# Kernel tuning notes

Hardware: AMD Instinct MI355X
Metric: run time of the kernel (lower is better)

## Reference

```python
import jax, jax.numpy as jnp
import numpy as np

# Model constants (match init_kwargs / torchcde conventions)
B = 1024        # batch
L = 128         # number of spline knots (grid_points = 0..L-1)
C_IN = 8        # input_channels
HID = 64        # hidden_channels
MLP_H = 128     # CDEFunc hidden width
INIT_H = 20     # initial-network hidden width


def setup_inputs() -> dict:
    key = jax.random.key(0)
    ks = jax.random.split(key, 9)
    # cubic spline coeffs: (B, L-1, 4*C_IN) laid out as [a, b, c, d] per interval
    coeffs = jax.random.normal(ks[0], (B, L - 1, 4 * C_IN), dtype=jnp.float32) * 0.1
    # initial network: C_IN -> 20 -> HID (ReLU, then Tanh)
    Wi1 = jax.random.normal(ks[1], (C_IN, INIT_H), dtype=jnp.float32) / np.sqrt(C_IN)
    bi1 = jnp.zeros((INIT_H,), jnp.float32)
    Wi2 = jax.random.normal(ks[2], (INIT_H, HID), dtype=jnp.float32) / np.sqrt(INIT_H)
    bi2 = jnp.zeros((HID,), jnp.float32)
    # CDE vector field: (HID+1) -> 128 -> C_IN*HID (ReLU, then Tanh)
    W1 = jax.random.normal(ks[3], (HID + 1, MLP_H), dtype=jnp.float32) / np.sqrt(HID + 1)
    b1 = jnp.zeros((MLP_H,), jnp.float32)
    W2 = jax.random.normal(ks[4], (MLP_H, C_IN * HID), dtype=jnp.float32) / np.sqrt(MLP_H)
    b2 = jnp.zeros((C_IN * HID,), jnp.float32)
    return {"coeffs": coeffs, "Wi1": Wi1, "bi1": bi1, "Wi2": Wi2, "bi2": bi2,
            "W1": W1, "b1": b1, "W2": W2, "b2": b2}


def reference(coeffs, Wi1, bi1, Wi2, bi2, W1, b1, W2, b2):
    Lm1 = coeffs.shape[1]
    # a,b,c,d: each (B, L-1, C_IN). X(t) = a + b*f + c*f^2 + d*f^3 on interval idx,
    # dX/dt = b + 2c*f + 3d*f^2, with f = t - idx (torchcde CubicSpline convention).
    a, b, c, d = jnp.split(coeffs, 4, axis=-1)

    def dXdt(t):
        idx = jnp.clip(jnp.floor(t).astype(jnp.int32), 0, Lm1 - 1)
        fr = t - idx
        return b[:, idx] + 2.0 * c[:, idx] * fr + 3.0 * d[:, idx] * fr * fr  # (B, C_IN)

    def cde_func(t, z):
        # FFN([HID+1, 128, C_IN*HID], ReLU hidden, Tanh output) on concat(t, z)
        tz = jnp.concatenate([jnp.full((z.shape[0], 1), t, z.dtype), z], axis=1)
        h = jax.nn.relu(tz @ W1 + b1)
        return jnp.tanh(h @ W2 + b2).reshape(z.shape[0], HID, C_IN)  # (B, HID, C_IN)

    def vf(t, z):
        # dz/dt = f(t,z) @ dX/dt
        return jnp.einsum('bhc,bc->bh', cde_func(t, z), dXdt(t))

    # z0 = initial(X(t0)); X(0) = a at interval 0 with frac 0
    X0 = a[:, 0]
    z0 = jnp.tanh(jax.nn.relu(X0 @ Wi1 + bi1) @ Wi2 + bi2)  # (B, HID)

    def rk4_step(z, i):
        t = i.astype(z.dtype)
        k1 = vf(t, z)
        k2 = vf(t + 0.5, z + 0.5 * k1)
        k3 = vf(t + 0.5, z + 0.5 * k2)
        k4 = vf(t + 1.0, z + k3)
        z_new = z + (k1 + 2.0 * k2 + 2.0 * k3 + k4) / 6.0
        return z_new, z_new

    _, zs = jax.lax.scan(rk4_step, z0, jnp.arange(Lm1))  # (L-1, B, HID)
    # z evaluated at all grid points, like cdeint(t=X.grid_points): (B, L, HID)
    return jnp.concatenate([z0[None], zs], axis=0).transpose(1, 0, 2)
```

## Files before the change

kernel.cpp:

```cpp
#include <hip/hip_runtime.h>
#include <stdint.h>

#define LM1  127
#define NTHR 512

typedef _Float16 half8_t __attribute__((ext_vector_type(8)));
typedef _Float16 half4_t __attribute__((ext_vector_type(4)));
typedef float    f32x4   __attribute__((ext_vector_type(4)));

__device__ __forceinline__ float fast_tanh(float x) {
  float e = __expf(2.0f * x);
  return 1.0f - 2.0f * __builtin_amdgcn_rcpf(e + 1.0f);
}

#define BAR() asm volatile("s_waitcnt lgkmcnt(0)\n\ts_barrier" ::: "memory")

__global__ void __launch_bounds__(NTHR, 2) cde_kernel(
    const float* __restrict__ coeffs,
    const float* __restrict__ Wi1, const float* __restrict__ bi1,
    const float* __restrict__ Wi2, const float* __restrict__ bi2,
    const float* __restrict__ W1,  const float* __restrict__ b1,
    const float* __restrict__ W2,  const float* __restrict__ b2,
    float* __restrict__ out)
{
  __shared__ __align__(16) _Float16 zsbT[2][1024];
  __shared__ __align__(16) _Float16 hA[2048];
  __shared__ __align__(16) float    gds[2][3][4][8];

  const int t    = threadIdx.x;
  const int lane = t & 63;
  const int w    = t >> 6;
  const int l15  = lane & 15;
  const int lq   = lane >> 4;
  const int lqh  = lq >> 1, lql = lq & 1;
  const int r4   = l15 & 3;
  const bool rowok = (l15 < 4);
  const int row0 = blockIdx.x * 4;

  for (int u = t; u < 1024; u += NTHR) ((uint32_t*)zsbT)[u] = 0u;

  half8_t wA[2];
  #pragma unroll
  for (int kt = 0; kt < 2; ++kt)
    #pragma unroll
    for (int j = 0; j < 8; ++j)
      wA[kt][j] = (_Float16)W1[(1 + 32 * kt + 8 * lq + j) * 128 + 16 * w + l15];

  f32x4 w1t4, b14;
  #pragma unroll
  for (int reg = 0; reg < 4; ++reg) {
    w1t4[reg] = W1[16 * w + 4 * lq + reg];
    b14[reg]  = b1[16 * w + 4 * lq + reg];
  }

  half8_t wf[4][4];
  #pragma unroll
  for (int mt = 0; mt < 4; ++mt)
    #pragma unroll
    for (int kt = 0; kt < 4; ++kt)
      #pragma unroll
      for (int j = 0; j < 8; ++j)
        wf[mt][kt][j] =
            (_Float16)W2[(32 * kt + 8 * lq + j) * 512 + 64 * w + 16 * mt + l15];

  f32x4 b2v[4];
  #pragma unroll
  for (int mt = 0; mt < 4; ++mt)
    b2v[mt] = *(const f32x4*)&b2[64 * w + 16 * mt + 4 * lq];

  _Float16* const hwp = &hA[128 * (2 * w + lqh) + 8 * l15 + 4 * lql];
  const int zbase = 128 * w + 8 * l15;
  const int dA = 4 * lql + lqh;
  const int dB = 4 * lql + 2 + lqh;

  float z[4];
  {
    const float* cb = coeffs + (size_t)(row0 + r4) * (LM1 * 32);
    float x0[8];
    #pragma unroll
    for (int c = 0; c < 8; ++c) x0[c] = cb[c];
    float acc[4];
    #pragma unroll
    for (int mt = 0; mt < 4; ++mt) acc[mt] = bi2[8 * w + 2 * mt + lqh];
    for (int j = 0; j < 20; ++j) {
      float uj = bi1[j];
      #pragma unroll
      for (int c = 0; c < 8; ++c) uj += x0[c] * Wi1[c * 20 + j];
      uj = fmaxf(uj, 0.0f);
      #pragma unroll
      for (int mt = 0; mt < 4; ++mt) acc[mt] += uj * Wi2[j * 64 + 8 * w + 2 * mt + lqh];
    }
    #pragma unroll
    for (int mt = 0; mt < 4; ++mt) z[mt] = fast_tanh(acc[mt]);
  }
  if (rowok) {
    const float zA = lql ? z[2] : z[0];
    const float zB = lql ? z[3] : z[1];
    zsbT[0][zbase + dA] = (_Float16)zA;
    zsbT[0][zbase + dB] = (_Float16)zB;
    float* op = out + (size_t)(row0 + l15) * 8192 + 8 * w;
    op[dA] = zA;
    op[dB] = zB;
  }

  const int rg = (lane >> 3) & 3, cg = lane & 7;
  const float* cbp = coeffs + (size_t)(row0 + rg) * (LM1 * 32);
  float pb = 0.f, pc = 0.f, pd = 0.f, pbn = 0.f;
  const bool stg = (w == 7) && (lane < 32);
  if (stg) { pb = cbp[8 + cg]; pc = cbp[16 + cg]; pd = cbp[24 + cg]; pbn = cbp[40 + cg]; }

  __syncthreads();

  for (int i = 0; i < LM1; ++i) {
    if (stg) {
      gds[i & 1][0][rg][cg] = pb;
      gds[i & 1][1][rg][cg] = pb + pc + 0.75f * pd;
      gds[i & 1][2][rg][cg] = (i < LM1 - 1) ? pbn : fmaf(3.0f, pd, fmaf(2.0f, pc, pb));
      if (i + 1 < LM1) {
        const float* nb = cbp + (size_t)(i + 1) * 32;
        pb = nb[8 + cg]; pc = nb[16 + cg]; pd = nb[24 + cg];
        pbn = (i + 2 < LM1) ? nb[40 + cg] : 0.0f;
      }
    }

    float ksum[4] = {0.f, 0.f, 0.f, 0.f};
    #pragma unroll
    for (int s = 0; s < 4; ++s) {
      const int   rb = s & 1, wb = rb ^ 1;
      const int   gi = (s == 0) ? 0 : (s == 3) ? 2 : 1;
      const float ts = (float)i + ((s == 0) ? 0.0f : (s == 3) ? 1.0f : 0.5f);

      const half8_t zb0 = *(const half8_t*)(&zsbT[rb][8 * lane]);
      const half8_t zb1 = *(const half8_t*)(&zsbT[rb][512 + 8 * lane]);
      f32x4 hd = {0.f, 0.f, 0.f, 0.f};
      hd = __builtin_amdgcn_mfma_f32_16x16x32_f16(wA[0], zb0, hd, 0, 0, 0);
      hd = __builtin_amdgcn_mfma_f32_16x16x32_f16(wA[1], zb1, hd, 0, 0, 0);
      half4_t hv;
      hv[0] = (_Float16)fmaxf(hd.x + fmaf(ts, w1t4.x, b14.x), 0.0f);
      hv[1] = (_Float16)fmaxf(hd.y + fmaf(ts, w1t4.y, b14.y), 0.0f);
      hv[2] = (_Float16)fmaxf(hd.z + fmaf(ts, w1t4.z, b14.z), 0.0f);
      hv[3] = (_Float16)fmaxf(hd.w + fmaf(ts, w1t4.w, b14.w), 0.0f);
      *(half4_t*)hwp = hv;
      BAR();

      const f32x4 gv = *(const f32x4*)&gds[i & 1][gi][r4][4 * lql];
      half8_t hb[4];
      #pragma unroll
      for (int kt = 0; kt < 4; ++kt)
        hb[kt] = *(const half8_t*)(&hA[512 * kt + 8 * lane]);
      f32x4 d0 = {0.f, 0.f, 0.f, 0.f}, d1 = d0, d2 = d0, d3 = d0;
      #pragma unroll
      for (int kt = 0; kt < 4; ++kt) {
        d0 = __builtin_amdgcn_mfma_f32_16x16x32_f16(wf[0][kt], hb[kt], d0, 0, 0, 0);
        d1 = __builtin_amdgcn_mfma_f32_16x16x32_f16(wf[1][kt], hb[kt], d1, 0, 0, 0);
        d2 = __builtin_amdgcn_mfma_f32_16x16x32_f16(wf[2][kt], hb[kt], d2, 0, 0, 0);
        d3 = __builtin_amdgcn_mfma_f32_16x16x32_f16(wf[3][kt], hb[kt], d3, 0, 0, 0);
      }
      const float p0 = fast_tanh(d0.x + b2v[0].x) * gv.x + fast_tanh(d0.y + b2v[0].y) * gv.y
                     + fast_tanh(d0.z + b2v[0].z) * gv.z + fast_tanh(d0.w + b2v[0].w) * gv.w;
      const float p1 = fast_tanh(d1.x + b2v[1].x) * gv.x + fast_tanh(d1.y + b2v[1].y) * gv.y
                     + fast_tanh(d1.z + b2v[1].z) * gv.z + fast_tanh(d1.w + b2v[1].w) * gv.w;
      const float p2 = fast_tanh(d2.x + b2v[2].x) * gv.x + fast_tanh(d2.y + b2v[2].y) * gv.y
                     + fast_tanh(d2.z + b2v[2].z) * gv.z + fast_tanh(d2.w + b2v[2].w) * gv.w;
      const float p3 = fast_tanh(d3.x + b2v[3].x) * gv.x + fast_tanh(d3.y + b2v[3].y) * gv.y
                     + fast_tanh(d3.z + b2v[3].z) * gv.z + fast_tanh(d3.w + b2v[3].w) * gv.w;
      const float kcv0 = p0 + __shfl_xor(p0, 16, 64);
      const float kcv1 = p1 + __shfl_xor(p1, 16, 64);
      const float kcv2 = p2 + __shfl_xor(p2, 16, 64);
      const float kcv3 = p3 + __shfl_xor(p3, 16, 64);
      const float wgt = (s == 1 || s == 2) ? 2.0f : 1.0f;
      ksum[0] += wgt * kcv0;
      ksum[1] += wgt * kcv1;
      ksum[2] += wgt * kcv2;
      ksum[3] += wgt * kcv3;

      if (s < 3) {
        const float cn = (s == 2) ? 1.0f : 0.5f;
        if (rowok) {
          const float zA = lql ? z[2] : z[0], kA = lql ? kcv2 : kcv0;
          const float zB = lql ? z[3] : z[1], kB = lql ? kcv3 : kcv1;
          zsbT[wb][zbase + dA] = (_Float16)fmaf(cn, kA, zA);
          zsbT[wb][zbase + dB] = (_Float16)fmaf(cn, kB, zB);
        }
      } else {
        z[0] = fmaf(ksum[0], 1.0f / 6.0f, z[0]);
        z[1] = fmaf(ksum[1], 1.0f / 6.0f, z[1]);
        z[2] = fmaf(ksum[2], 1.0f / 6.0f, z[2]);
        z[3] = fmaf(ksum[3], 1.0f / 6.0f, z[3]);
        if (rowok) {
          const float zA = lql ? z[2] : z[0];
          const float zB = lql ? z[3] : z[1];
          zsbT[wb][zbase + dA] = (_Float16)zA;
          zsbT[wb][zbase + dB] = (_Float16)zB;
          float* op = out + (size_t)(row0 + l15) * 8192 + (size_t)(i + 1) * 64 + 8 * w;
          op[dA] = zA;
          op[dB] = zB;
        }
      }
      BAR();
    }
  }
}

extern "C" void kernel_launch(void* const* d_in, const int* in_sizes, int n_in,
                              void* d_out, int out_size, void* d_ws, size_t ws_size,
                              hipStream_t stream) {
  const float* coeffs = (const float*)d_in[0];
  const float* Wi1    = (const float*)d_in[1];
  const float* bi1    = (const float*)d_in[2];
  const float* Wi2    = (const float*)d_in[3];
  const float* bi2    = (const float*)d_in[4];
  const float* W1     = (const float*)d_in[5];
  const float* b1     = (const float*)d_in[6];
  const float* W2     = (const float*)d_in[7];
  const float* b2     = (const float*)d_in[8];
  float* out          = (float*)d_out;
  (void)in_sizes; (void)n_in; (void)out_size; (void)d_ws; (void)ws_size;
  cde_kernel<<<256, NTHR, 0, stream>>>(coeffs, Wi1, bi1, Wi2, bi2,
                                       W1, b1, W2, b2, out);
}
```

Before: 605.0 us.

## Halve block to 4 waves, compute full hidden layer per wave to drop mid-stage barrier

Shrinks the block from 8 to 4 waves and has each wave compute the whole 128-wide first MLP layer redundantly into a private LDS buffer. This removes one of the two block barriers per RK stage. Each wave now owns 128 output columns of the second layer (8 MFMA tiles instead of 4), and spline-coefficient staging moves to the end of the last stage. The cost is redundant first-layer MFMA work, much higher register pressure from holding 8x2 plus 8x4 weight fragments, and fewer waves for latency hiding, with launch bounds dropped to 1 block.

```diff
diff --git a/kernel.cpp b/kernel.cpp
--- a/kernel.cpp
+++ b/kernel.cpp
@@ -2,7 +2,7 @@
 #include <stdint.h>
 
 #define LM1  127
-#define NTHR 512
+#define NTHR 256
 
 typedef _Float16 half8_t __attribute__((ext_vector_type(8)));
 typedef _Float16 half4_t __attribute__((ext_vector_type(4)));
@@ -15,7 +15,7 @@
 
 #define BAR() asm volatile("s_waitcnt lgkmcnt(0)\n\ts_barrier" ::: "memory")
 
-__global__ void __launch_bounds__(NTHR, 2) cde_kernel(
+__global__ void __launch_bounds__(NTHR, 1) cde_kernel(
     const float* __restrict__ coeffs,
     const float* __restrict__ Wi1, const float* __restrict__ bi1,
     const float* __restrict__ Wi2, const float* __restrict__ bi2,
@@ -24,7 +24,7 @@
     float* __restrict__ out)
 {
   __shared__ __align__(16) _Float16 zsbT[2][1024];
-  __shared__ __align__(16) _Float16 hA[2048];
+  __shared__ __align__(16) _Float16 hA[4][2048];
   __shared__ __align__(16) float    gds[2][3][4][8];
 
   const int t    = threadIdx.x;
@@ -34,96 +34,106 @@
   const int lq   = lane >> 4;
   const int lqh  = lq >> 1, lql = lq & 1;
   const int r4   = l15 & 3;
-  const bool rowok = (l15 < 4);
+  const bool owner = (l15 < 4) && (lql == 0);
   const int row0 = blockIdx.x * 4;
 
   for (int u = t; u < 1024; u += NTHR) ((uint32_t*)zsbT)[u] = 0u;
 
-  half8_t wA[2];
-  #pragma unroll
-  for (int kt = 0; kt < 2; ++kt)
-    #pragma unroll
-    for (int j = 0; j < 8; ++j)
-      wA[kt][j] = (_Float16)W1[(1 + 32 * kt + 8 * lq + j) * 128 + 16 * w + l15];
-
-  f32x4 w1t4, b14;
-  #pragma unroll
-  for (int reg = 0; reg < 4; ++reg) {
-    w1t4[reg] = W1[16 * w + 4 * lq + reg];
-    b14[reg]  = b1[16 * w + 4 * lq + reg];
-  }
-
-  half8_t wf[4][4];
-  #pragma unroll
-  for (int mt = 0; mt < 4; ++mt)
+  half8_t wA[8][2];
+  #pragma unroll
+  for (int m = 0; m < 8; ++m)
+    #pragma unroll
+    for (int kt = 0; kt < 2; ++kt)
+      #pragma unroll
+      for (int j = 0; j < 8; ++j)
+        wA[m][kt][j] = (_Float16)W1[(1 + 32 * kt + 8 * lq + j) * 128 + 16 * m + l15];
+
+  f32x4 w1t4[8], b14[8];
+  #pragma unroll
+  for (int m = 0; m < 8; ++m)
+    #pragma unroll
+    for (int reg = 0; reg < 4; ++reg) {
+      w1t4[m][reg] = W1[16 * m + 4 * lq + reg];
+      b14[m][reg]  = b1[16 * m + 4 * lq + reg];
+    }
+
+  half8_t wf[8][4];
+  #pragma unroll
+  for (int mt = 0; mt < 8; ++mt)
     #pragma unroll
     for (int kt = 0; kt < 4; ++kt)
       #pragma unroll
       for (int j = 0; j < 8; ++j)
         wf[mt][kt][j] =
-            (_Float16)W2[(32 * kt + 8 * lq + j) * 512 + 64 * w + 16 * mt + l15];
-
-  f32x4 b2v[4];
-  #pragma unroll
-  for (int mt = 0; mt < 4; ++mt)
-    b2v[mt] = *(const f32x4*)&b2[64 * w + 16 * mt + 4 * lq];
-
-  _Float16* const hwp = &hA[128 * (2 * w + lqh) + 8 * l15 + 4 * lql];
-  const int zbase = 128 * w + 8 * l15;
-  const int dA = 4 * lql + lqh;
-  const int dB = 4 * lql + 2 + lqh;
-
-  float z[4];
+            (_Float16)W2[(32 * kt + 8 * lq + j) * 512 + 128 * w + 16 * mt + l15];
+
+  f32x4 b2v[8];
+  #pragma unroll
+  for (int mt = 0; mt < 8; ++mt)
+    b2v[mt] = *(const f32x4*)&b2[128 * w + 16 * mt + 4 * lq];
+
+  _Float16* const hAp = &hA[w][0];
+  const int hbase = 8 * l15 + 4 * lql + 128 * lqh;
+
+  int zoffs[8];
+  #pragma unroll
+  for (int mt = 0; mt < 8; ++mt) {
+    const int h = 16 * w + 2 * mt + lqh;
+    zoffs[mt] = 512 * (h >> 5) + 128 * ((h >> 3) & 3) + 8 * l15 + (h & 7);
+  }
+
+  float z[8];
   {
     const float* cb = coeffs + (size_t)(row0 + r4) * (LM1 * 32);
     float x0[8];
     #pragma unroll
     for (int c = 0; c < 8; ++c) x0[c] = cb[c];
-    float acc[4];
-    #pragma unroll
-    for (int mt = 0; mt < 4; ++mt) acc[mt] = bi2[8 * w + 2 * mt + lqh];
+    float acc[8];
+    #pragma unroll
+    for (int mt = 0; mt < 8; ++mt) acc[mt] = bi2[16 * w + 2 * mt + lqh];
     for (int j = 0; j < 20; ++j) {
       float uj = bi1[j];
       #pragma unroll
       for (int c = 0; c < 8; ++c) uj += x0[c] * Wi1[c * 20 + j];
       uj = fmaxf(uj, 0.0f);
       #pragma unroll
-      for (int mt = 0; mt < 4; ++mt) acc[mt] += uj * Wi2[j * 64 + 8 * w + 2 * mt + lqh];
-    }
-    #pragma unroll
-    for (int mt = 0; mt < 4; ++mt) z[mt] = fast_tanh(acc[mt]);
-  }
-  if (rowok) {
-    const float zA = lql ? z[2] : z[0];
-    const float zB = lql ? z[3] : z[1];
-    zsbT[0][zbase + dA] = (_Float16)zA;
-    zsbT[0][zbase + dB] = (_Float16)zB;
-    float* op = out + (size_t)(row0 + l15) * 8192 + 8 * w;
-    op[dA] = zA;
-    op[dB] = zB;
+      for (int mt = 0; mt < 8; ++mt) acc[mt] += uj * Wi2[j * 64 + 16 * w + 2 * mt + lqh];
+    }
+    #pragma unroll
+    for (int mt = 0; mt < 8; ++mt) z[mt] = fast_tanh(acc[mt]);
+  }
+  if (owner) {
+    #pragma unroll
+    for (int mt = 0; mt < 8; ++mt) {
+      zsbT[0][zoffs[mt]] = (_Float16)z[mt];
+      out[(size_t)(row0 + l15) * 8192 + 16 * w + 2 * mt + lqh] = z[mt];
+    }
   }
 
   const int rg = (lane >> 3) & 3, cg = lane & 7;
   const float* cbp = coeffs + (size_t)(row0 + rg) * (LM1 * 32);
-  float pb = 0.f, pc = 0.f, pd = 0.f, pbn = 0.f;
-  const bool stg = (w == 7) && (lane < 32);
-  if (stg) { pb = cbp[8 + cg]; pc = cbp[16 + cg]; pd = cbp[24 + cg]; pbn = cbp[40 + cg]; }
+  const bool stg = (w == 3) && (lane < 32);
+  float pb2 = 0.f, pc2 = 0.f, pd2 = 0.f, pbn2 = 0.f;
+  if (stg) {
+    const float pb = cbp[8 + cg], pc = cbp[16 + cg], pd = cbp[24 + cg], pbn = cbp[40 + cg];
+    gds[0][0][rg][cg] = pb;
+    gds[0][1][rg][cg] = pb + pc + 0.75f * pd;
+    gds[0][2][rg][cg] = pbn;
+  }
 
   __syncthreads();
 
   for (int i = 0; i < LM1; ++i) {
-    if (stg) {
-      gds[i & 1][0][rg][cg] = pb;
-      gds[i & 1][1][rg][cg] = pb + pc + 0.75f * pd;
-      gds[i & 1][2][rg][cg] = (i < LM1 - 1) ? pbn : fmaf(3.0f, pd, fmaf(2.0f, pc, pb));
-      if (i + 1 < LM1) {
-        const float* nb = cbp + (size_t)(i + 1) * 32;
-        pb = nb[8 + cg]; pc = nb[16 + cg]; pd = nb[24 + cg];
-        pbn = (i + 2 < LM1) ? nb[40 + cg] : 0.0f;
-      }
-    }
-
-    float ksum[4] = {0.f, 0.f, 0.f, 0.f};
+    if (stg && i + 1 < LM1) {
+      const float* nb = cbp + (size_t)(i + 1) * 32;
+      pb2 = nb[8 + cg]; pc2 = nb[16 + cg]; pd2 = nb[24 + cg];
+      pbn2 = (i + 2 < LM1) ? nb[40 + cg] : 0.0f;
+    }
+
+    float ksum[8];
+    #pragma unroll
+    for (int mt = 0; mt < 8; ++mt) ksum[mt] = 0.0f;
+
     #pragma unroll
     for (int s = 0; s < 4; ++s) {
       const int   rb = s & 1, wb = rb ^ 1;
@@ -132,70 +142,62 @@
 
       const half8_t zb0 = *(const half8_t*)(&zsbT[rb][8 * lane]);
       const half8_t zb1 = *(const half8_t*)(&zsbT[rb][512 + 8 * lane]);
-      f32x4 hd = {0.f, 0.f, 0.f, 0.f};
-      hd = __builtin_amdgcn_mfma_f32_16x16x32_f16(wA[0], zb0, hd, 0, 0, 0);
-      hd = __builtin_amdgcn_mfma_f32_16x16x32_f16(wA[1], zb1, hd, 0, 0, 0);
-      half4_t hv;
-      hv[0] = (_Float16)fmaxf(hd.x + fmaf(ts, w1t4.x, b14.x), 0.0f);
-      hv[1] = (_Float16)fmaxf(hd.y + fmaf(ts, w1t4.y, b14.y), 0.0f);
-      hv[2] = (_Float16)fmaxf(hd.z + fmaf(ts, w1t4.z, b14.z), 0.0f);
-      hv[3] = (_Float16)fmaxf(hd.w + fmaf(ts, w1t4.w, b14.w), 0.0f);
-      *(half4_t*)hwp = hv;
-      BAR();
-
       const f32x4 gv = *(const f32x4*)&gds[i & 1][gi][r4][4 * lql];
+
+      #pragma unroll
+      for (int m = 0; m < 8; ++m) {
+        f32x4 hd = {0.f, 0.f, 0.f, 0.f};
+        hd = __builtin_amdgcn_mfma_f32_16x16x32_f16(wA[m][0], zb0, hd, 0, 0, 0);
+        hd = __builtin_amdgcn_mfma_f32_16x16x32_f16(wA[m][1], zb1, hd, 0, 0, 0);
+        half4_t hv;
+        hv[0] = (_Float16)fmaxf(hd.x + fmaf(ts, w1t4[m].x, b14[m].x), 0.0f);
+        hv[1] = (_Float16)fmaxf(hd.y + fmaf(ts, w1t4[m].y, b14[m].y), 0.0f);
+        hv[2] = (_Float16)fmaxf(hd.z + fmaf(ts, w1t4[m].z, b14[m].z), 0.0f);
+        hv[3] = (_Float16)fmaxf(hd.w + fmaf(ts, w1t4[m].w, b14[m].w), 0.0f);
+        *(half4_t*)(hAp + hbase + 256 * m) = hv;
+      }
+      asm volatile("s_waitcnt lgkmcnt(0)" ::: "memory");
+
       half8_t hb[4];
       #pragma unroll
       for (int kt = 0; kt < 4; ++kt)
-        hb[kt] = *(const half8_t*)(&hA[512 * kt + 8 * lane]);
-      f32x4 d0 = {0.f, 0.f, 0.f, 0.f}, d1 = d0, d2 = d0, d3 = d0;
-      #pragma unroll
-      for (int kt = 0; kt < 4; ++kt) {
-        d0 = __builtin_amdgcn_mfma_f32_16x16x32_f16(wf[0][kt], hb[kt], d0, 0, 0, 0);
-        d1 = __builtin_amdgcn_mfma_f32_16x16x32_f16(wf[1][kt], hb[kt], d1, 0, 0, 0);
-        d2 = __builtin_amdgcn_mfma_f32_16x16x32_f16(wf[2][kt], hb[kt], d2, 0, 0, 0);
-        d3 = __builtin_amdgcn_mfma_f32_16x16x32_f16(wf[3][kt], hb[kt], d3, 0, 0, 0);
+        hb[kt] = *(const half8_t*)(hAp + 512 * kt + 8 * lane);
+      f32x4 d[8];
+      #pragma unroll
+      for (int mt = 0; mt < 8; ++mt) d[mt] = (f32x4){0.f, 0.f, 0.f, 0.f};
+      #pragma unroll
+      for (int kt = 0; kt < 4; ++kt)
+        #pragma unroll
+        for (int mt = 0; mt < 8; ++mt)
+          d[mt] = __builtin_amdgcn_mfma_f32_16x16x32_f16(wf[mt][kt], hb[kt], d[mt], 0, 0, 0);
+
+      const float wgt = (s == 1 || s == 2) ? 2.0f : 1.0f;
+      const float cn  = (s == 2) ? 1.0f : 0.5f;
+      #pragma unroll
+      for (int mt = 0; mt < 8; ++mt) {
+        float p = fast_tanh(d[mt].x + b2v[mt].x) * gv.x
+                + fast_tanh(d[mt].y + b2v[mt].y) * gv.y
+                + fast_tanh(d[mt].z + b2v[mt].z) * gv.z
+                + fast_tanh(d[mt].w + b2v[mt].w) * gv.w;
+        const float kcv = p + __shfl_xor(p, 16, 64);
+        ksum[mt] += wgt * kcv;
+        if (s < 3) {
+          if (owner) zsbT[wb][zoffs[mt]] = (_Float16)fmaf(cn, kcv, z[mt]);
+        } else {
+          z[mt] = fmaf(ksum[mt], 1.0f / 6.0f, z[mt]);
+          if (owner) {
+            zsbT[wb][zoffs[mt]] = (_Float16)z[mt];
+            out[(size_t)(row0 + l15) * 8192 + (size_t)(i + 1) * 64
+                + 16 * w + 2 * mt + lqh] = z[mt];
+          }
+        }
       }
-      const float p0 = fast_tanh(d0.x + b2v[0].x) * gv.x + fast_tanh(d0.y + b2v[0].y) * gv.y
-                     + fast_tanh(d0.z + b2v[0].z) * gv.z + fast_tanh(d0.w + b2v[0].w) * gv.w;
-      const float p1 = fast_tanh(d1.x + b2v[1].x) * gv.x + fast_tanh(d1.y + b2v[1].y) * gv.y
-                     + fast_tanh(d1.z + b2v[1].z) * gv.z + fast_tanh(d1.w + b2v[1].w) * gv.w;
-      const float p2 = fast_tanh(d2.x + b2v[2].x) * gv.x + fast_tanh(d2.y + b2v[2].y) * gv.y
-                     + fast_tanh(d2.z + b2v[2].z) * gv.z + fast_tanh(d2.w + b2v[2].w) * gv.w;
-      const float p3 = fast_tanh(d3.x + b2v[3].x) * gv.x + fast_tanh(d3.y + b2v[3].y) * gv.y
-                     + fast_tanh(d3.z + b2v[3].z) * gv.z + fast_tanh(d3.w + b2v[3].w) * gv.w;
-      const float kcv0 = p0 + __shfl_xor(p0, 16, 64);
-      const float kcv1 = p1 + __shfl_xor(p1, 16, 64);
-      const float kcv2 = p2 + __shfl_xor(p2, 16, 64);
-      const float kcv3 = p3 + __shfl_xor(p3, 16, 64);
-      const float wgt = (s == 1 || s == 2) ? 2.0f : 1.0f;
-      ksum[0] += wgt * kcv0;
-      ksum[1] += wgt * kcv1;
-      ksum[2] += wgt * kcv2;
-      ksum[3] += wgt * kcv3;
-
-      if (s < 3) {
-        const float cn = (s == 2) ? 1.0f : 0.5f;
-        if (rowok) {
-          const float zA = lql ? z[2] : z[0], kA = lql ? kcv2 : kcv0;
-          const float zB = lql ? z[3] : z[1], kB = lql ? kcv3 : kcv1;
-          zsbT[wb][zbase + dA] = (_Float16)fmaf(cn, kA, zA);
-          zsbT[wb][zbase + dB] = (_Float16)fmaf(cn, kB, zB);
-        }
-      } else {
-        z[0] = fmaf(ksum[0], 1.0f / 6.0f, z[0]);
-        z[1] = fmaf(ksum[1], 1.0f / 6.0f, z[1]);
-        z[2] = fmaf(ksum[2], 1.0f / 6.0f, z[2]);
-        z[3] = fmaf(ksum[3], 1.0f / 6.0f, z[3]);
-        if (rowok) {
-          const float zA = lql ? z[2] : z[0];
-          const float zB = lql ? z[3] : z[1];
-          zsbT[wb][zbase + dA] = (_Float16)zA;
-          zsbT[wb][zbase + dB] = (_Float16)zB;
-          float* op = out + (size_t)(row0 + l15) * 8192 + (size_t)(i + 1) * 64 + 8 * w;
-          op[dA] = zA;
-          op[dB] = zB;
-        }
+      if (s == 3 && stg && i + 1 < LM1) {
+        const int ii = i + 1;
+        gds[ii & 1][0][rg][cg] = pb2;
+        gds[ii & 1][1][rg][cg] = pb2 + pc2 + 0.75f * pd2;
+        gds[ii & 1][2][rg][cg] =
+            (ii < LM1 - 1) ? pbn2 : fmaf(3.0f, pd2, fmaf(2.0f, pc2, pb2));
       }
       BAR();
     }
```

After: 1.125 ms. +85.9%, slower.
